# Kernel tuning notes

Hardware: AMD Instinct MI355X
Metric: run time of the kernel (lower is better)

The kernel has to match this reference:

```python
import jax, jax.numpy as jnp
import numpy as np

B, N, C_IN = 32, 1024, 128
F0, F1, F2 = 64, 64, 64
OUT = 10
RATIOS = (0.8, 0.8)
EPS = 1e-5


def setup_inputs() -> dict:
    key = jax.random.key(0)
    ks = jax.random.split(key, 16)
    N_nodes = jax.random.randint(ks[0], (B,), N // 2, N + 1)
    mask = (jnp.arange(N)[None, :] < N_nodes[:, None]).astype(jnp.float32)
    x = jax.random.normal(ks[1], (B, N, C_IN), dtype=jnp.float32)
    # sparse-ish symmetric binary adjacency restricted to valid nodes
    A = (jax.random.uniform(ks[2], (B, N, N)) < 0.02).astype(jnp.float32)
    A = jnp.maximum(A, jnp.swapaxes(A, 1, 2))
    A = A * mask[:, :, None] * mask[:, None, :]
    def lin(k, fi, fo):
        b = 1.0 / np.sqrt(fi)
        kw, kb = jax.random.split(k)
        return (jax.random.uniform(kw, (fi, fo), minval=-b, maxval=b),
                jax.random.uniform(kb, (fo,), minval=-b, maxval=b))
    W0, b0 = lin(ks[3], C_IN, F0)
    W1, b1 = lin(ks[4], F0, F1)
    W2, b2 = lin(ks[5], F1, F2)
    bp0 = 1.0 / np.sqrt(F0)
    p0 = jax.random.uniform(ks[6], (F0, 1), minval=-bp0, maxval=bp0)
    bp1 = 1.0 / np.sqrt(F1)
    p1 = jax.random.uniform(ks[7], (F1, 1), minval=-bp1, maxval=bp1)
    Wfc, bfc = lin(ks[8], F2, OUT)
    return {"x": x, "A": A, "mask": mask, "N_nodes": N_nodes,
            "W0": W0, "b0": b0, "W1": W1, "b1": b1, "W2": W2, "b2": b2,
            "p0": p0, "p1": p1, "Wfc": Wfc, "bfc": bfc}


def _gconv(x, A, W, b):
    # Kipf-Welling normalized Laplacian conv, batched dense
    n = A.shape[1]
    A_hat = A + jnp.eye(n, dtype=A.dtype)[None]
    D = (jnp.sum(A_hat, axis=1) + EPS) ** -0.5  # [B,N]
    L = D[:, :, None] * A_hat * D[:, None, :]
    h = jnp.einsum('bnm,bmc->bnc', L, x) @ W + b
    return jax.nn.relu(h)


def _pool(x, A, mask, N_nodes, p, ratio):
    Bc, Nc, C = x.shape
    y = (x.reshape(Bc * Nc, C) @ p).reshape(Bc, Nc)
    y = y / jnp.sqrt(jnp.sum(p ** 2))
    N_remove = (N_nodes.astype(jnp.float32) * (1.0 - ratio)).astype(N_nodes.dtype)
    # remove the N_remove lowest-scoring valid nodes per graph
    y_eff = jnp.where(mask > 0, y, jnp.inf)
    ranks = jnp.argsort(jnp.argsort(y_eff, axis=1), axis=1)  # ascending rank
    new_mask = mask * (ranks >= N_remove[:, None]).astype(mask.dtype)
    x = x * jnp.tanh(y)[:, :, None] * new_mask[:, :, None]
    A = new_mask[:, :, None] * A * new_mask[:, None, :]
    return x, A, new_mask, N_nodes - N_remove


def reference(x, A, mask, N_nodes, W0, b0, W1, b1, W2, b2, p0, p1, Wfc, bfc):
    x = _gconv(x, A, W0, b0)
    x, A, mask, N_nodes = _pool(x, A, mask, N_nodes, p0, RATIOS[0])
    x = _gconv(x, A, W1, b1)
    x, A, mask, N_nodes = _pool(x, A, mask, N_nodes, p1, RATIOS[1])
    x = _gconv(x, A, W2, b2)
    x = jnp.max(x, axis=1)  # global max pool over nodes [B,F2]
    return x @ Wfc + bfc
```

## Files before the change

kernel.cpp:

```cpp
#include <hip/hip_runtime.h>
#include <cstdint>
#include <cstddef>

#define BB 32
#define NN 1024
#define CIN 128
#define FF 64
#define NOUT 10
#define CAP 128
#define EPSV 1e-5f

typedef float vf4 __attribute__((ext_vector_type(4)));
__device__ __forceinline__ float4 ldnt(const float4* p) {
    vf4 v = __builtin_nontemporal_load((const vf4*)p);
    return make_float4(v.x, v.y, v.z, v.w);
}

__global__ __launch_bounds__(256) void k_front(const float* __restrict__ A,
                                               const float* __restrict__ x,
                                               const float* __restrict__ W0,
                                               const int* __restrict__ Nn,
                                               const float* __restrict__ b2f,
                                               float* __restrict__ gmax,
                                               unsigned short* __restrict__ adj,
                                               int* __restrict__ cnt,
                                               float* __restrict__ c1,
                                               float* __restrict__ c2,
                                               float* __restrict__ T) {
    __shared__ __align__(16) float Wl[64 * 64];
    int tid = threadIdx.x;
    int wave = tid >> 6, lane = tid & 63;
    if (blockIdx.x >= 10240) {
        for (int i = tid; i < BB * 64; i += 256)
            gmax[i] = fmaxf(b2f[i & 63], 0.f);
        return;
    }
    if (blockIdx.x >= 8192) {
        int gid = blockIdx.x - 8192;
        int b = gid & 31;
        int cch = gid >> 5;
        if (cch * 16 >= Nn[b]) return;
        int row0 = (b << 10) + cch * 16;
        int rsub = lane >> 4, f0 = (lane & 15) * 4;
        int r = row0 + wave * 4 + rsub;
        const float4* xr = (const float4*)(x + (size_t)r * CIN);
        float4 acc = {0.f, 0.f, 0.f, 0.f};
#pragma unroll
        for (int kc = 0; kc < 2; ++kc) {
            if (kc) __syncthreads();
            for (int t = tid; t < 64 * 16; t += 256)
                ((float4*)Wl)[t] = ((const float4*)W0)[kc * 1024 + t];
            __syncthreads();
#pragma unroll 4
            for (int k4 = 0; k4 < 16; ++k4) {
                float4 xv = ldnt(xr + kc * 16 + k4);
                float4 w0 = *(const float4*)&Wl[(k4 * 4 + 0) * 64 + f0];
                float4 w1 = *(const float4*)&Wl[(k4 * 4 + 1) * 64 + f0];
                float4 w2 = *(const float4*)&Wl[(k4 * 4 + 2) * 64 + f0];
                float4 w3 = *(const float4*)&Wl[(k4 * 4 + 3) * 64 + f0];
                acc.x += xv.x * w0.x; acc.y += xv.x * w0.y; acc.z += xv.x * w0.z; acc.w += xv.x * w0.w;
                acc.x += xv.y * w1.x; acc.y += xv.y * w1.y; acc.z += xv.y * w1.z; acc.w += xv.y * w1.w;
                acc.x += xv.z * w2.x; acc.y += xv.z * w2.y; acc.z += xv.z * w2.z; acc.w += xv.z * w2.w;
                acc.x += xv.w * w3.x; acc.y += xv.w * w3.y; acc.z += xv.w * w3.z; acc.w += xv.w * w3.w;
            }
        }
        *(float4*)&T[(size_t)r * 64 + f0] = acc;
    } else {
        int r = blockIdx.x * 4 + wave;
        int b = r >> 10;
        int Nb = Nn[b];
        int rl = r & 1023;
        if (rl >= Nb) {
            if (lane == 0) {
                cnt[r] = 0;
                float D = 1.0f / sqrtf(1.0f + EPSV);
                c1[r] = D;
                c2[r] = D * D;
            }
            return;
        }
        unsigned short* adjs = ((unsigned short*)Wl) + wave * CAP;
        const float4* Arow = (const float4*)(A + (size_t)r * NN);
        int nch = (Nb + 255) >> 8;
        float4 z4 = {0.f, 0.f, 0.f, 0.f};
        float4 v0 = ldnt(Arow + lane);
        float4 v1 = ldnt(Arow + 64 + lane);
        float4 v2 = (nch > 2) ? ldnt(Arow + 128 + lane) : z4;
        float4 v3 = (nch > 3) ? ldnt(Arow + 192 + lane) : z4;
        int c = 0;
        unsigned long long lt = (lane == 0) ? 0ULL : ((1ULL << lane) - 1ULL);
        float4 vv[4] = {v0, v1, v2, v3};
#pragma unroll
        for (int it = 0; it < 4; ++it) {
            float4 v = vv[it];
            int j0 = it * 256 + lane * 4;
            unsigned long long m0 = __ballot(v.x != 0.f);
            unsigned long long m1 = __ballot(v.y != 0.f);
            unsigned long long m2 = __ballot(v.z != 0.f);
            unsigned long long m3 = __ballot(v.w != 0.f);
            int before = __popcll(m0 & lt) + __popcll(m1 & lt) +
                         __popcll(m2 & lt) + __popcll(m3 & lt);
            int p = c + before;
            if (v.x != 0.f) { if (p < CAP) adjs[p] = (unsigned short)(j0 + 0); ++p; }
            if (v.y != 0.f) { if (p < CAP) adjs[p] = (unsigned short)(j0 + 1); ++p; }
            if (v.z != 0.f) { if (p < CAP) adjs[p] = (unsigned short)(j0 + 2); ++p; }
            if (v.w != 0.f) { if (p < CAP) adjs[p] = (unsigned short)(j0 + 3); ++p; }
            c += __popcll(m0) + __popcll(m1) + __popcll(m2) + __popcll(m3);
        }
        int cc = (c > CAP) ? CAP : c;
        uint32_t* dst = (uint32_t*)(adj + (size_t)r * CAP);
        if (lane * 2 < cc) dst[lane] = ((const uint32_t*)adjs)[lane];
        if (lane == 0) {
            cnt[r] = cc;
            float D = 1.0f / sqrtf((float)c + 1.0f + EPSV);
            c1[r] = D;
            c2[r] = D * D;
        }
    }
}

__global__ __launch_bounds__(256) void k_mid(const unsigned short* __restrict__ adj,
                                             const int* __restrict__ cnt,
                                             const float* __restrict__ nm,
                                             float* __restrict__ c1, float* __restrict__ c2,
                                             const float* __restrict__ Xin,
                                             const float* __restrict__ W,
                                             const float* __restrict__ y,
                                             float* __restrict__ T,
                                             const int* __restrict__ Nn) {
    __shared__ __align__(16) float Wl[64 * 64];
    int tid = threadIdx.x;
    if (blockIdx.x >= 8192) {
        int gid = blockIdx.x - 8192;
        int b = gid & 31;
        int cch = gid >> 5;
        if (cch * 16 >= Nn[b]) return;
        int row0 = (b << 10) + cch * 16;
        for (int t = tid; t < 64 * 16; t += 256)
            ((float4*)Wl)[t] = ((const float4*)W)[t];
        __syncthreads();
        int wave = tid >> 6, lane = tid & 63;
        int rsub = lane >> 4, f0 = (lane & 15) * 4;
        int r = row0 + wave * 4 + rsub;
        float sc = tanhf(y[r]) * nm[r];
        const float4* xr = (const float4*)(Xin + (size_t)r * 64);
        float4 acc = {0.f, 0.f, 0.f, 0.f};
#pragma unroll 4
        for (int k4 = 0; k4 < 16; ++k4) {
            float4 xv = ldnt(xr + k4);
            float4 w0 = *(const float4*)&Wl[(k4 * 4 + 0) * 64 + f0];
            float4 w1 = *(const float4*)&Wl[(k4 * 4 + 1) * 64 + f0];
            float4 w2 = *(const float4*)&Wl[(k4 * 4 + 2) * 64 + f0];
            float4 w3 = *(const float4*)&Wl[(k4 * 4 + 3) * 64 + f0];
            acc.x += xv.x * w0.x; acc.y += xv.x * w0.y; acc.z += xv.x * w0.z; acc.w += xv.x * w0.w;
            acc.x += xv.y * w1.x; acc.y += xv.y * w1.y; acc.z += xv.y * w1.z; acc.w += xv.y * w1.w;
            acc.x += xv.z * w2.x; acc.y += xv.z * w2.y; acc.z += xv.z * w2.z; acc.w += xv.z * w2.w;
            acc.x += xv.w * w3.x; acc.y += xv.w * w3.y; acc.z += xv.w * w3.z; acc.w += xv.w * w3.w;
        }
        acc.x *= sc; acc.y *= sc; acc.z *= sc; acc.w *= sc;
        *(float4*)&T[(size_t)r * 64 + f0] = acc;
    } else {
        int wave = tid >> 6, lane = tid & 63;
        int r = blockIdx.x * 4 + wave;
        int b = r >> 10;
        if ((r & 1023) >= Nn[b]) return;
        float m = nm[r];
        if (m == 0.f) {
            if (lane == 0) c1[r] = 0.f;
            return;
        }
        const unsigned short* arow = adj + (size_t)r * CAP;
        const float* nmb = nm + (b << 10);
        int n = cnt[r];
        float s = 0.f;
        if (lane < n)      s  = nmb[arow[lane]];
        if (lane + 64 < n) s += nmb[arow[lane + 64]];
        for (int sh = 32; sh; sh >>= 1) s += __shfl_xor(s, sh, 64);
        if (lane == 0) {
            float D = 1.0f / sqrtf(m * s + 1.0f + EPSV);
            c1[r] = m * D;
            c2[r] = D * D;
        }
    }
}

__global__ __launch_bounds__(256) void k_spmm(const unsigned short* __restrict__ adj,
                                              const int* __restrict__ cnt,
                                              const float* __restrict__ c1,
                                              const float* __restrict__ c2,
                                              const float* __restrict__ T,
                                              const float* __restrict__ bias,
                                              float* __restrict__ X,
                                              const float* __restrict__ p,
                                              float* __restrict__ y,
                                              float* __restrict__ gmax,
                                              const int* __restrict__ Nn) {
    __shared__ __align__(16) float c1s[NN];
    __shared__ float red[4][64];
    int b   = blockIdx.x & 31;
    int cch = blockIdx.x >> 5;
    int Nb = Nn[b];
    if (cch * 16 >= Nb) return;
    int tid = threadIdx.x;
    int n4 = (Nb + 3) >> 2;
    if (tid < n4) ((float4*)c1s)[tid] = ((const float4*)(c1 + (b << 10)))[tid];
    __syncthreads();
    int wave = tid >> 6, lane = tid & 63;
    int r0 = (b << 10) + cch * 16 + wave * 4;
    const float* Tb = T + ((size_t)(b << 10) << 6);
    float bv = bias[lane];
    float pv = 0.f, ppinv = 0.f;
    if (p != nullptr) {
        pv = p[lane];
        float pp = pv * pv;
        for (int s = 32; s; s >>= 1) pp += __shfl_xor(pp, s, 64);
        ppinv = 1.0f / sqrtf(pp);
    }
    float vmax = 0.f;
#pragma unroll
    for (int rr = 0; rr < 4; ++rr) {
        int r = r0 + rr;
        int rl = r & 1023;
        if (rl >= Nb) break;
        if (c1s[rl] == 0.f) continue;
        const unsigned short* arow = adj + (size_t)r * CAP;
        int n = cnt[r];
        float acc0 = 0.f, acc1 = 0.f, acc2 = 0.f, acc3 = 0.f;
        int t = 0;
        for (; t + 4 <= n; t += 4) {
            ushort4 j4 = *(const ushort4*)(arow + t);
            acc0 += c1s[j4.x] * Tb[((int)j4.x << 6) + lane];
            acc1 += c1s[j4.y] * Tb[((int)j4.y << 6) + lane];
            acc2 += c1s[j4.z] * Tb[((int)j4.z << 6) + lane];
            acc3 += c1s[j4.w] * Tb[((int)j4.w << 6) + lane];
        }
        for (; t < n; ++t) {
            int j = arow[t];
            acc0 += c1s[j] * Tb[(j << 6) + lane];
        }
        float acc = (acc0 + acc1) + (acc2 + acc3);
        float o = c1s[rl] * acc + c2[r] * T[((size_t)r << 6) + lane] + bv;
        o = fmaxf(o, 0.f);
        if (X != nullptr) X[((size_t)r << 6) + lane] = o;
        if (p != nullptr) {
            float a = o * pv;
            for (int s = 32; s; s >>= 1) a += __shfl_xor(a, s, 64);
            if (lane == 0) y[r] = a * ppinv;
        }
        vmax = fmaxf(vmax, o);
    }
    if (gmax != nullptr) {
        red[wave][lane] = vmax;
        __syncthreads();
        if (wave == 0) {
            float m = fmaxf(fmaxf(red[0][lane], red[1][lane]),
                            fmaxf(red[2][lane], red[3][lane]));
            atomicMax((int*)&gmax[(b << 6) + lane], __float_as_int(m));
        }
    }
}

__global__ __launch_bounds__(256) void k_rank(const float* __restrict__ y,
                                              const float* __restrict__ maskSrc,
                                              const int* __restrict__ nsrc,
                                              const int* __restrict__ nbound,
                                              float* __restrict__ nmOut,
                                              int* __restrict__ ncur) {
    __shared__ __align__(16) float yv[NN];
    int b = blockIdx.x >> 4;
    int sub = blockIdx.x & 15;
    int tid = threadIdx.x;
    const float INF = __builtin_inff();
    int Nb = nbound[b];
    if ((sub << 6) >= Nb) return;
    {
        float4 v;
        if (tid * 4 < Nb) {
            v = ((const float4*)(y + (b << 10)))[tid];
            float4 m = ((const float4*)(maskSrc + (b << 10)))[tid];
            v.x = (m.x > 0.f) ? v.x : INF;
            v.y = (m.y > 0.f) ? v.y : INF;
            v.z = (m.z > 0.f) ? v.z : INF;
            v.w = (m.w > 0.f) ? v.w : INF;
        } else {
            v.x = INF; v.y = INF; v.z = INF; v.w = INF;
        }
        ((float4*)yv)[tid] = v;
    }
    int n = nsrc[b];
    const float RM = (float)(1.0 - 0.8);
    int nrem = (int)((float)n * RM);
    if (sub == 0 && tid == 0) ncur[b] = n - nrem;
    __syncthreads();
    int i = (sub << 6) + (tid >> 2);
    int q = tid & 3;
    float yi = yv[i];
    int rank = 0;
    if (yi < INF) {
        const float4* jbase = (const float4*)yv + (q << 6);
        int j0 = q << 8;
        int tend = (Nb - j0 + 3) >> 2;
        if (tend > 64) tend = 64;
#pragma unroll 8
        for (int t = 0; t < tend; ++t) {
            float4 a = jbase[t];
            int j = j0 + t * 4;
            rank += (a.x < yi || (a.x == yi && j     < i)) ? 1 : 0;
            rank += (a.y < yi || (a.y == yi && j + 1 < i)) ? 1 : 0;
            rank += (a.z < yi || (a.z == yi && j + 2 < i)) ? 1 : 0;
            rank += (a.w < yi || (a.w == yi && j + 3 < i)) ? 1 : 0;
        }
    }
    rank += __shfl_xor(rank, 1, 64);
    rank += __shfl_xor(rank, 2, 64);
    if (q == 0) {
        float nmv = (yi < INF && rank >= nrem) ? 1.f : 0.f;
        nmOut[(b << 10) + i] = nmv;
    }
}

__global__ __launch_bounds__(64) void k_fc(const float* __restrict__ gmax,
                                           const float* __restrict__ Wfc,
                                           const float* __restrict__ bfc,
                                           float* __restrict__ out) {
    __shared__ float gl[64];
    int b = blockIdx.x, lane = threadIdx.x;
    gl[lane] = gmax[(b << 6) + lane];
    __syncthreads();
    if (lane < NOUT) {
        float acc = bfc[lane];
        for (int k = 0; k < 64; ++k) acc += gl[k] * Wfc[k * NOUT + lane];
        out[b * NOUT + lane] = acc;
    }
}

extern "C" void kernel_launch(void* const* d_in, const int* in_sizes, int n_in,
                              void* d_out, int out_size, void* d_ws, size_t ws_size,
                              hipStream_t stream) {
    const float* x    = (const float*)d_in[0];
    const float* A    = (const float*)d_in[1];
    const float* mask = (const float*)d_in[2];
    const int*   Nn   = (const int*)d_in[3];
    const float* W0   = (const float*)d_in[4];
    const float* b0   = (const float*)d_in[5];
    const float* W1   = (const float*)d_in[6];
    const float* b1   = (const float*)d_in[7];
    const float* W2   = (const float*)d_in[8];
    const float* b2   = (const float*)d_in[9];
    const float* p0   = (const float*)d_in[10];
    const float* p1   = (const float*)d_in[11];
    const float* Wfc  = (const float*)d_in[12];
    const float* bfc  = (const float*)d_in[13];
    float* out = (float*)d_out;

    char* ws = (char*)d_ws;
    size_t off = 0;
    auto alloc = [&](size_t bytes) -> void* {
        void* p = ws + off;
        off = (off + bytes + 255) & ~(size_t)255;
        return p;
    };
    unsigned short* adj = (unsigned short*)alloc((size_t)BB * NN * CAP * 2);
    int*   cnt  = (int*)  alloc((size_t)BB * NN * 4);
    float* X    = (float*)alloc((size_t)BB * NN * 64 * 4);
    float* T    = (float*)alloc((size_t)BB * NN * 64 * 4);
    float* c1   = (float*)alloc((size_t)BB * NN * 4);
    float* c2   = (float*)alloc((size_t)BB * NN * 4);
    float* y    = (float*)alloc((size_t)BB * NN * 4);
    float* nm0  = (float*)alloc((size_t)BB * NN * 4);
    float* nm1  = (float*)alloc((size_t)BB * NN * 4);
    int*   nc0  = (int*)  alloc((size_t)BB * 4);
    int*   nc1  = (int*)  alloc((size_t)BB * 4);
    float* gmax = (float*)alloc((size_t)BB * 64 * 4);

    k_front<<<8192 + 2048 + 1, 256, 0, stream>>>(A, x, W0, Nn, b2, gmax,
                                                 adj, cnt, c1, c2, T);
    k_spmm<<<2048, 256, 0, stream>>>(adj, cnt, c1, c2, T, b0, X, p0, y, nullptr, Nn);
    k_rank<<<BB * 16, 256, 0, stream>>>(y, mask, Nn, Nn, nm0, nc0);
    k_mid<<<8192 + 2048, 256, 0, stream>>>(adj, cnt, nm0, c1, c2, X, W1, y, T, Nn);
    k_spmm<<<2048, 256, 0, stream>>>(adj, cnt, c1, c2, T, b1, X, p1, y, nullptr, Nn);
    k_rank<<<BB * 16, 256, 0, stream>>>(y, nm0, nc0, Nn, nm1, nc1);
    k_mid<<<8192 + 2048, 256, 0, stream>>>(adj, cnt, nm1, c1, c2, X, W2, y, T, Nn);
    k_spmm<<<2048, 256, 0, stream>>>(adj, cnt, c1, c2, T, b2, nullptr, nullptr, nullptr,
                                     gmax, Nn);
    k_fc<<<BB, 64, 0, stream>>>(gmax, Wfc, bfc, out);
}
```

Measured before the change: 355.1 us.

## Fuse rank and FC into spmm via last-block-per-graph atomic counter

Removes the separate k_rank and k_fc launches. Each k_spmm block now bumps a per-graph counter, and the last block to finish for a graph computes the top-k mask or the final FC layer in place. Ranking switches to packed 64-bit sortable keys with a single block doing an O(N^2) comparison per graph, where the old k_rank spread this over 16 blocks. This saves launch gaps but serialises the ranking work onto one block per graph.

```diff
diff --git a/kernel.cpp b/kernel.cpp
--- a/kernel.cpp
+++ b/kernel.cpp
@@ -26,13 +26,15 @@
                                                int* __restrict__ cnt,
                                                float* __restrict__ c1,
                                                float* __restrict__ c2,
-                                               float* __restrict__ T) {
+                                               float* __restrict__ T,
+                                               int* __restrict__ ctrs) {
     __shared__ __align__(16) float Wl[64 * 64];
     int tid = threadIdx.x;
     int wave = tid >> 6, lane = tid & 63;
     if (blockIdx.x >= 10240) {
         for (int i = tid; i < BB * 64; i += 256)
             gmax[i] = fmaxf(b2f[i & 63], 0.f);
+        if (tid < 96) ctrs[tid] = 0;
         return;
     }
     if (blockIdx.x >= 8192) {
@@ -194,9 +196,19 @@
                                               const float* __restrict__ p,
                                               float* __restrict__ y,
                                               float* __restrict__ gmax,
-                                              const int* __restrict__ Nn) {
+                                              const int* __restrict__ Nn,
+                                              const float* __restrict__ maskSrc,
+                                              const int* __restrict__ nsrc,
+                                              float* __restrict__ nmOut,
+                                              int* __restrict__ ncur,
+                                              const float* __restrict__ Wfc,
+                                              const float* __restrict__ bfc,
+                                              float* __restrict__ outP,
+                                              int* __restrict__ ctr) {
     __shared__ __align__(16) float c1s[NN];
+    __shared__ __align__(16) unsigned long long kv[NN];
     __shared__ float red[4][64];
+    __shared__ int islast;
     int b   = blockIdx.x & 31;
     int cch = blockIdx.x >> 5;
     int Nb = Nn[b];
@@ -258,79 +270,77 @@
             atomicMax((int*)&gmax[(b << 6) + lane], __float_as_int(m));
         }
     }
-}
-
-__global__ __launch_bounds__(256) void k_rank(const float* __restrict__ y,
-                                              const float* __restrict__ maskSrc,
-                                              const int* __restrict__ nsrc,
-                                              const int* __restrict__ nbound,
-                                              float* __restrict__ nmOut,
-                                              int* __restrict__ ncur) {
-    __shared__ __align__(16) float yv[NN];
-    int b = blockIdx.x >> 4;
-    int sub = blockIdx.x & 15;
-    int tid = threadIdx.x;
+    __syncthreads();
+    if (tid == 0) {
+        __threadfence();
+        int target = (Nb + 15) >> 4;
+        int old = __hip_atomic_fetch_add(&ctr[b], 1, __ATOMIC_ACQ_REL,
+                                         __HIP_MEMORY_SCOPE_AGENT);
+        islast = (old == target - 1);
+    }
+    __syncthreads();
+    if (!islast) return;
+    __threadfence();
     const float INF = __builtin_inff();
-    int Nb = nbound[b];
-    if ((sub << 6) >= Nb) return;
-    {
-        float4 v;
-        if (tid * 4 < Nb) {
-            v = ((const float4*)(y + (b << 10)))[tid];
-            float4 m = ((const float4*)(maskSrc + (b << 10)))[tid];
-            v.x = (m.x > 0.f) ? v.x : INF;
-            v.y = (m.y > 0.f) ? v.y : INF;
-            v.z = (m.z > 0.f) ? v.z : INF;
-            v.w = (m.w > 0.f) ? v.w : INF;
-        } else {
-            v.x = INF; v.y = INF; v.z = INF; v.w = INF;
-        }
-        ((float4*)yv)[tid] = v;
-    }
-    int n = nsrc[b];
-    const float RM = (float)(1.0 - 0.8);
-    int nrem = (int)((float)n * RM);
-    if (sub == 0 && tid == 0) ncur[b] = n - nrem;
-    __syncthreads();
-    int i = (sub << 6) + (tid >> 2);
-    int q = tid & 3;
-    float yi = yv[i];
-    int rank = 0;
-    if (yi < INF) {
-        const float4* jbase = (const float4*)yv + (q << 6);
-        int j0 = q << 8;
-        int tend = (Nb - j0 + 3) >> 2;
-        if (tend > 64) tend = 64;
-#pragma unroll 8
-        for (int t = 0; t < tend; ++t) {
-            float4 a = jbase[t];
-            int j = j0 + t * 4;
-            rank += (a.x < yi || (a.x == yi && j     < i)) ? 1 : 0;
-            rank += (a.y < yi || (a.y == yi && j + 1 < i)) ? 1 : 0;
-            rank += (a.z < yi || (a.z == yi && j + 2 < i)) ? 1 : 0;
-            rank += (a.w < yi || (a.w == yi && j + 3 < i)) ? 1 : 0;
-        }
-    }
-    rank += __shfl_xor(rank, 1, 64);
-    rank += __shfl_xor(rank, 2, 64);
-    if (q == 0) {
-        float nmv = (yi < INF && rank >= nrem) ? 1.f : 0.f;
-        nmOut[(b << 10) + i] = nmv;
-    }
-}
-
-__global__ __launch_bounds__(64) void k_fc(const float* __restrict__ gmax,
-                                           const float* __restrict__ Wfc,
-                                           const float* __restrict__ bfc,
-                                           float* __restrict__ out) {
-    __shared__ float gl[64];
-    int b = blockIdx.x, lane = threadIdx.x;
-    gl[lane] = gmax[(b << 6) + lane];
-    __syncthreads();
-    if (lane < NOUT) {
-        float acc = bfc[lane];
-        for (int k = 0; k < 64; ++k) acc += gl[k] * Wfc[k * NOUT + lane];
-        out[b * NOUT + lane] = acc;
+    if (nmOut != nullptr) {
+        float* yv = c1s;
+        {
+            float4 v;
+            if (tid * 4 < Nb) {
+                v = ((const float4*)(y + (b << 10)))[tid];
+                float4 m = ((const float4*)(maskSrc + (b << 10)))[tid];
+                v.x = (m.x > 0.f) ? v.x : INF;
+                v.y = (m.y > 0.f) ? v.y : INF;
+                v.z = (m.z > 0.f) ? v.z : INF;
+                v.w = (m.w > 0.f) ? v.w : INF;
+            } else {
+                v.x = INF; v.y = INF; v.z = INF; v.w = INF;
+            }
+            ((float4*)yv)[tid] = v;
+        }
+        int n = nsrc[b];
+        const float RM = (float)(1.0 - 0.8);
+        int nrem = (int)((float)n * RM);
+        if (tid == 0) ncur[b] = n - nrem;
+        __syncthreads();
+#pragma unroll
+        for (int t = 0; t < 4; ++t) {
+            int i = tid + (t << 8);
+            unsigned int u = __float_as_uint(yv[i]);
+            u ^= (unsigned int)((int)u >> 31) | 0x80000000u;
+            kv[i] = ((unsigned long long)u << 10) | (unsigned int)i;
+        }
+        __syncthreads();
+        unsigned long long k0 = kv[tid], k1 = kv[tid + 256],
+                           k2 = kv[tid + 512], k3 = kv[tid + 768];
+        int r0k = 0, r1k = 0, r2k = 0, r3k = 0;
+        int nkc = (Nb + 1) >> 1;
+#pragma unroll 4
+        for (int c = 0; c < nkc; ++c) {
+            ulonglong2 a = ((const ulonglong2*)kv)[c];
+            r0k += (a.x < k0) + (a.y < k0);
+            r1k += (a.x < k1) + (a.y < k1);
+            r2k += (a.x < k2) + (a.y < k2);
+            r3k += (a.x < k3) + (a.y < k3);
+        }
+        int rk[4] = {r0k, r1k, r2k, r3k};
+#pragma unroll
+        for (int t = 0; t < 4; ++t) {
+            int i = tid + (t << 8);
+            nmOut[(b << 10) + i] = (yv[i] < INF && rk[t] >= nrem) ? 1.f : 0.f;
+        }
+    } else if (outP != nullptr) {
+        float* gl = c1s;
+        if (tid < 64)
+            gl[tid] = __uint_as_float(__hip_atomic_load(
+                (unsigned int*)&gmax[(b << 6) + tid],
+                __ATOMIC_RELAXED, __HIP_MEMORY_SCOPE_AGENT));
+        __syncthreads();
+        if (tid < NOUT) {
+            float acc = bfc[tid];
+            for (int k = 0; k < 64; ++k) acc += gl[k] * Wfc[k * NOUT + tid];
+            outP[b * NOUT + tid] = acc;
+        }
     }
 }
 
@@ -372,16 +382,20 @@
     int*   nc0  = (int*)  alloc((size_t)BB * 4);
     int*   nc1  = (int*)  alloc((size_t)BB * 4);
     float* gmax = (float*)alloc((size_t)BB * 64 * 4);
+    int*   ctrs = (int*)  alloc(96 * 4);
 
     k_front<<<8192 + 2048 + 1, 256, 0, stream>>>(A, x, W0, Nn, b2, gmax,
-                                                 adj, cnt, c1, c2, T);
-    k_spmm<<<2048, 256, 0, stream>>>(adj, cnt, c1, c2, T, b0, X, p0, y, nullptr, Nn);
-    k_rank<<<BB * 16, 256, 0, stream>>>(y, mask, Nn, Nn, nm0, nc0);
+                                                 adj, cnt, c1, c2, T, ctrs);
+    k_spmm<<<2048, 256, 0, stream>>>(adj, cnt, c1, c2, T, b0, X, p0, y, nullptr, Nn,
+                                     mask, Nn, nm0, nc0,
+                                     nullptr, nullptr, nullptr, ctrs);
     k_mid<<<8192 + 2048, 256, 0, stream>>>(adj, cnt, nm0, c1, c2, X, W1, y, T, Nn);
-    k_spmm<<<2048, 256, 0, stream>>>(adj, cnt, c1, c2, T, b1, X, p1, y, nullptr, Nn);
-    k_rank<<<BB * 16, 256, 0, stream>>>(y, nm0, nc0, Nn, nm1, nc1);
+    k_spmm<<<2048, 256, 0, stream>>>(adj, cnt, c1, c2, T, b1, X, p1, y, nullptr, Nn,
+                                     nm0, nc0, nm1, nc1,
+                                     nullptr, nullptr, nullptr, ctrs + 32);
     k_mid<<<8192 + 2048, 256, 0, stream>>>(adj, cnt, nm1, c1, c2, X, W2, y, T, Nn);
     k_spmm<<<2048, 256, 0, stream>>>(adj, cnt, c1, c2, T, b2, nullptr, nullptr, nullptr,
-                                     gmax, Nn);
-    k_fc<<<BB, 64, 0, stream>>>(gmax, Wfc, bfc, out);
+                                     gmax, Nn,
+                                     nullptr, nullptr, nullptr, nullptr,
+                                     Wfc, bfc, out, ctrs + 64);
 }
```

New measurement: 566.4 us. +59.5%, slower.

## Fuse rank and mask-degree computation into GEMM kernel, defer tanh scaling to SpMM

Applied to the files above, without the earlier changes.

The separate pooling rank kernel is merged with the degree/normalisation pass and launched in the same grid as the feature GEMM, which removes two kernel launches and their dependency stalls. Each rank block now recomputes ranks for the whole graph using packed 64-bit (key, index) comparisons, so it can build the new mask in shared memory for neighbour degree sums. The tanh(y)·mask scaling is no longer applied to T in the GEMM but per-neighbour inside the SpMM gather. The cost is redundant rank work across the sixteen sub-blocks of each graph and extra shared-memory loads and multiplies in the SpMM inner loop.

```diff
diff --git a/kernel.cpp b/kernel.cpp
--- a/kernel.cpp
+++ b/kernel.cpp
@@ -119,19 +119,120 @@
     }
 }
 
-__global__ __launch_bounds__(256) void k_mid(const unsigned short* __restrict__ adj,
-                                             const int* __restrict__ cnt,
-                                             const float* __restrict__ nm,
-                                             float* __restrict__ c1, float* __restrict__ c2,
-                                             const float* __restrict__ Xin,
-                                             const float* __restrict__ W,
-                                             const float* __restrict__ y,
-                                             float* __restrict__ T,
-                                             const int* __restrict__ Nn) {
-    __shared__ __align__(16) float Wl[64 * 64];
+template<int DEFER>
+__global__ __launch_bounds__(256) void k_spmm(const unsigned short* __restrict__ adj,
+                                              const int* __restrict__ cnt,
+                                              const float* __restrict__ c1,
+                                              const float* __restrict__ c2,
+                                              const float* __restrict__ T,
+                                              const float* __restrict__ bias,
+                                              float* __restrict__ X,
+                                              const float* __restrict__ p,
+                                              float* __restrict__ y,
+                                              float* __restrict__ gmax,
+                                              const int* __restrict__ Nn,
+                                              const float* __restrict__ scs) {
+    __shared__ __align__(16) float c1s[NN];
+    __shared__ __align__(16) float scss[DEFER ? NN : 4];
+    __shared__ float red[4][64];
+    int b   = blockIdx.x & 31;
+    int cch = blockIdx.x >> 5;
+    int Nb = Nn[b];
+    if (cch * 16 >= Nb) return;
     int tid = threadIdx.x;
-    if (blockIdx.x >= 8192) {
-        int gid = blockIdx.x - 8192;
+    int n4 = (Nb + 3) >> 2;
+    if (tid < n4) {
+        ((float4*)c1s)[tid] = ((const float4*)(c1 + (b << 10)))[tid];
+        if (DEFER)
+            ((float4*)scss)[tid] = ((const float4*)(scs + (b << 10)))[tid];
+    }
+    __syncthreads();
+    int wave = tid >> 6, lane = tid & 63;
+    int r0 = (b << 10) + cch * 16 + wave * 4;
+    const float* Tb = T + ((size_t)(b << 10) << 6);
+    float bv = bias[lane];
+    float pv = 0.f, ppinv = 0.f;
+    if (p != nullptr) {
+        pv = p[lane];
+        float pp = pv * pv;
+        for (int s = 32; s; s >>= 1) pp += __shfl_xor(pp, s, 64);
+        ppinv = 1.0f / sqrtf(pp);
+    }
+    float vmax = 0.f;
+#pragma unroll
+    for (int rr = 0; rr < 4; ++rr) {
+        int r = r0 + rr;
+        int rl = r & 1023;
+        if (rl >= Nb) break;
+        if (DEFER && c1s[rl] == 0.f) continue;
+        const unsigned short* arow = adj + (size_t)r * CAP;
+        int n = cnt[r];
+        float acc0 = 0.f, acc1 = 0.f, acc2 = 0.f, acc3 = 0.f;
+        int t = 0;
+        for (; t + 4 <= n; t += 4) {
+            ushort4 j4 = *(const ushort4*)(arow + t);
+            float t0 = Tb[((int)j4.x << 6) + lane];
+            float t1 = Tb[((int)j4.y << 6) + lane];
+            float t2 = Tb[((int)j4.z << 6) + lane];
+            float t3 = Tb[((int)j4.w << 6) + lane];
+            if (DEFER) {
+                t0 *= scss[j4.x]; t1 *= scss[j4.y];
+                t2 *= scss[j4.z]; t3 *= scss[j4.w];
+            }
+            acc0 += c1s[j4.x] * t0;
+            acc1 += c1s[j4.y] * t1;
+            acc2 += c1s[j4.z] * t2;
+            acc3 += c1s[j4.w] * t3;
+        }
+        for (; t < n; ++t) {
+            int j = arow[t];
+            float tv = Tb[(j << 6) + lane];
+            if (DEFER) tv *= scss[j];
+            acc0 += c1s[j] * tv;
+        }
+        float acc = (acc0 + acc1) + (acc2 + acc3);
+        float selfT = T[((size_t)r << 6) + lane];
+        if (DEFER) selfT = scss[rl] * selfT;
+        float o = c1s[rl] * acc + c2[r] * selfT + bv;
+        o = fmaxf(o, 0.f);
+        if (X != nullptr) X[((size_t)r << 6) + lane] = o;
+        if (p != nullptr) {
+            float a = o * pv;
+            for (int s = 32; s; s >>= 1) a += __shfl_xor(a, s, 64);
+            if (lane == 0) y[r] = a * ppinv;
+        }
+        vmax = fmaxf(vmax, o);
+    }
+    if (gmax != nullptr) {
+        red[wave][lane] = vmax;
+        __syncthreads();
+        if (wave == 0) {
+            float m = fmaxf(fmaxf(red[0][lane], red[1][lane]),
+                            fmaxf(red[2][lane], red[3][lane]));
+            atomicMax((int*)&gmax[(b << 6) + lane], __float_as_int(m));
+        }
+    }
+}
+
+__global__ __launch_bounds__(256) void k_rankgemm(const float* __restrict__ y,
+                                                  const float* __restrict__ maskSrc,
+                                                  const int* __restrict__ nsrc,
+                                                  const int* __restrict__ Nn,
+                                                  const unsigned short* __restrict__ adj,
+                                                  const int* __restrict__ cnt,
+                                                  const float* __restrict__ Xin,
+                                                  const float* __restrict__ W,
+                                                  float* __restrict__ nmOut,
+                                                  int* __restrict__ ncur,
+                                                  float* __restrict__ c1o,
+                                                  float* __restrict__ c2o,
+                                                  float* __restrict__ scso,
+                                                  float* __restrict__ T) {
+    __shared__ __align__(16) char smem[16384];
+    int tid = threadIdx.x;
+    if (blockIdx.x >= 512) {
+        float* Wl = (float*)smem;
+        int gid = blockIdx.x - 512;
         int b = gid & 31;
         int cch = gid >> 5;
         if (cch * 16 >= Nn[b]) return;
@@ -142,7 +243,6 @@
         int wave = tid >> 6, lane = tid & 63;
         int rsub = lane >> 4, f0 = (lane & 15) * 4;
         int r = row0 + wave * 4 + rsub;
-        float sc = tanhf(y[r]) * nm[r];
         const float4* xr = (const float4*)(Xin + (size_t)r * 64);
         float4 acc = {0.f, 0.f, 0.f, 0.f};
 #pragma unroll 4
@@ -157,165 +257,93 @@
             acc.x += xv.z * w2.x; acc.y += xv.z * w2.y; acc.z += xv.z * w2.z; acc.w += xv.z * w2.w;
             acc.x += xv.w * w3.x; acc.y += xv.w * w3.y; acc.z += xv.w * w3.z; acc.w += xv.w * w3.w;
         }
-        acc.x *= sc; acc.y *= sc; acc.z *= sc; acc.w *= sc;
         *(float4*)&T[(size_t)r * 64 + f0] = acc;
     } else {
+        float* yv = (float*)smem;
+        unsigned long long* kv = (unsigned long long*)(smem + 4096);
+        float* nml = (float*)(smem + 12288);
+        int b = blockIdx.x >> 4;
+        int sub = blockIdx.x & 15;
+        const float INF = __builtin_inff();
+        int Nb = Nn[b];
+        if ((sub << 6) >= Nb) return;
+        {
+            float4 v;
+            if (tid * 4 < Nb) {
+                v = ((const float4*)(y + (b << 10)))[tid];
+                float4 m = ((const float4*)(maskSrc + (b << 10)))[tid];
+                v.x = (m.x > 0.f) ? v.x : INF;
+                v.y = (m.y > 0.f) ? v.y : INF;
+                v.z = (m.z > 0.f) ? v.z : INF;
+                v.w = (m.w > 0.f) ? v.w : INF;
+            } else {
+                v.x = INF; v.y = INF; v.z = INF; v.w = INF;
+            }
+            ((float4*)yv)[tid] = v;
+        }
+        int n = nsrc[b];
+        const float RM = (float)(1.0 - 0.8);
+        int nrem = (int)((float)n * RM);
+        if (sub == 0 && tid == 0) ncur[b] = n - nrem;
+        __syncthreads();
+#pragma unroll
+        for (int t = 0; t < 4; ++t) {
+            int i = tid + (t << 8);
+            unsigned int u = __float_as_uint(yv[i]);
+            u ^= (unsigned int)((int)u >> 31) | 0x80000000u;
+            kv[i] = ((unsigned long long)u << 10) | (unsigned int)i;
+        }
+        __syncthreads();
+        unsigned long long k0 = kv[tid], k1 = kv[tid + 256],
+                           k2 = kv[tid + 512], k3 = kv[tid + 768];
+        int r0 = 0, r1 = 0, r2 = 0, r3 = 0;
+        int nkc = (Nb + 1) >> 1;
+#pragma unroll 4
+        for (int c = 0; c < nkc; ++c) {
+            ulonglong2 a = ((const ulonglong2*)kv)[c];
+            r0 += (a.x < k0) + (a.y < k0);
+            r1 += (a.x < k1) + (a.y < k1);
+            r2 += (a.x < k2) + (a.y < k2);
+            r3 += (a.x < k3) + (a.y < k3);
+        }
+        int rk[4] = {r0, r1, r2, r3};
+#pragma unroll
+        for (int t = 0; t < 4; ++t) {
+            int i = tid + (t << 8);
+            nml[i] = (yv[i] < INF && rk[t] >= nrem) ? 1.f : 0.f;
+        }
+        __syncthreads();
         int wave = tid >> 6, lane = tid & 63;
-        int r = blockIdx.x * 4 + wave;
-        int b = r >> 10;
-        if ((r & 1023) >= Nn[b]) return;
-        float m = nm[r];
-        if (m == 0.f) {
-            if (lane == 0) c1[r] = 0.f;
-            return;
-        }
-        const unsigned short* arow = adj + (size_t)r * CAP;
-        const float* nmb = nm + (b << 10);
-        int n = cnt[r];
-        float s = 0.f;
-        if (lane < n)      s  = nmb[arow[lane]];
-        if (lane + 64 < n) s += nmb[arow[lane + 64]];
-        for (int sh = 32; sh; sh >>= 1) s += __shfl_xor(s, sh, 64);
-        if (lane == 0) {
-            float D = 1.0f / sqrtf(m * s + 1.0f + EPSV);
-            c1[r] = m * D;
-            c2[r] = D * D;
-        }
-    }
-}
-
-__global__ __launch_bounds__(256) void k_spmm(const unsigned short* __restrict__ adj,
-                                              const int* __restrict__ cnt,
-                                              const float* __restrict__ c1,
-                                              const float* __restrict__ c2,
-                                              const float* __restrict__ T,
-                                              const float* __restrict__ bias,
-                                              float* __restrict__ X,
-                                              const float* __restrict__ p,
-                                              float* __restrict__ y,
-                                              float* __restrict__ gmax,
-                                              const int* __restrict__ Nn) {
-    __shared__ __align__(16) float c1s[NN];
-    __shared__ float red[4][64];
-    int b   = blockIdx.x & 31;
-    int cch = blockIdx.x >> 5;
-    int Nb = Nn[b];
-    if (cch * 16 >= Nb) return;
-    int tid = threadIdx.x;
-    int n4 = (Nb + 3) >> 2;
-    if (tid < n4) ((float4*)c1s)[tid] = ((const float4*)(c1 + (b << 10)))[tid];
-    __syncthreads();
-    int wave = tid >> 6, lane = tid & 63;
-    int r0 = (b << 10) + cch * 16 + wave * 4;
-    const float* Tb = T + ((size_t)(b << 10) << 6);
-    float bv = bias[lane];
-    float pv = 0.f, ppinv = 0.f;
-    if (p != nullptr) {
-        pv = p[lane];
-        float pp = pv * pv;
-        for (int s = 32; s; s >>= 1) pp += __shfl_xor(pp, s, 64);
-        ppinv = 1.0f / sqrtf(pp);
-    }
-    float vmax = 0.f;
-#pragma unroll
-    for (int rr = 0; rr < 4; ++rr) {
-        int r = r0 + rr;
-        int rl = r & 1023;
-        if (rl >= Nb) break;
-        if (c1s[rl] == 0.f) continue;
-        const unsigned short* arow = adj + (size_t)r * CAP;
-        int n = cnt[r];
-        float acc0 = 0.f, acc1 = 0.f, acc2 = 0.f, acc3 = 0.f;
-        int t = 0;
-        for (; t + 4 <= n; t += 4) {
-            ushort4 j4 = *(const ushort4*)(arow + t);
-            acc0 += c1s[j4.x] * Tb[((int)j4.x << 6) + lane];
-            acc1 += c1s[j4.y] * Tb[((int)j4.y << 6) + lane];
-            acc2 += c1s[j4.z] * Tb[((int)j4.z << 6) + lane];
-            acc3 += c1s[j4.w] * Tb[((int)j4.w << 6) + lane];
-        }
-        for (; t < n; ++t) {
-            int j = arow[t];
-            acc0 += c1s[j] * Tb[(j << 6) + lane];
-        }
-        float acc = (acc0 + acc1) + (acc2 + acc3);
-        float o = c1s[rl] * acc + c2[r] * T[((size_t)r << 6) + lane] + bv;
-        o = fmaxf(o, 0.f);
-        if (X != nullptr) X[((size_t)r << 6) + lane] = o;
-        if (p != nullptr) {
-            float a = o * pv;
-            for (int s = 32; s; s >>= 1) a += __shfl_xor(a, s, 64);
-            if (lane == 0) y[r] = a * ppinv;
-        }
-        vmax = fmaxf(vmax, o);
-    }
-    if (gmax != nullptr) {
-        red[wave][lane] = vmax;
-        __syncthreads();
-        if (wave == 0) {
-            float m = fmaxf(fmaxf(red[0][lane], red[1][lane]),
-                            fmaxf(red[2][lane], red[3][lane]));
-            atomicMax((int*)&gmax[(b << 6) + lane], __float_as_int(m));
-        }
-    }
-}
-
-__global__ __launch_bounds__(256) void k_rank(const float* __restrict__ y,
-                                              const float* __restrict__ maskSrc,
-                                              const int* __restrict__ nsrc,
-                                              const int* __restrict__ nbound,
-                                              float* __restrict__ nmOut,
-                                              int* __restrict__ ncur) {
-    __shared__ __align__(16) float yv[NN];
-    int b = blockIdx.x >> 4;
-    int sub = blockIdx.x & 15;
-    int tid = threadIdx.x;
-    const float INF = __builtin_inff();
-    int Nb = nbound[b];
-    if ((sub << 6) >= Nb) return;
-    {
-        float4 v;
-        if (tid * 4 < Nb) {
-            v = ((const float4*)(y + (b << 10)))[tid];
-            float4 m = ((const float4*)(maskSrc + (b << 10)))[tid];
-            v.x = (m.x > 0.f) ? v.x : INF;
-            v.y = (m.y > 0.f) ? v.y : INF;
-            v.z = (m.z > 0.f) ? v.z : INF;
-            v.w = (m.w > 0.f) ? v.w : INF;
-        } else {
-            v.x = INF; v.y = INF; v.z = INF; v.w = INF;
-        }
-        ((float4*)yv)[tid] = v;
-    }
-    int n = nsrc[b];
-    const float RM = (float)(1.0 - 0.8);
-    int nrem = (int)((float)n * RM);
-    if (sub == 0 && tid == 0) ncur[b] = n - nrem;
-    __syncthreads();
-    int i = (sub << 6) + (tid >> 2);
-    int q = tid & 3;
-    float yi = yv[i];
-    int rank = 0;
-    if (yi < INF) {
-        const float4* jbase = (const float4*)yv + (q << 6);
-        int j0 = q << 8;
-        int tend = (Nb - j0 + 3) >> 2;
-        if (tend > 64) tend = 64;
-#pragma unroll 8
-        for (int t = 0; t < tend; ++t) {
-            float4 a = jbase[t];
-            int j = j0 + t * 4;
-            rank += (a.x < yi || (a.x == yi && j     < i)) ? 1 : 0;
-            rank += (a.y < yi || (a.y == yi && j + 1 < i)) ? 1 : 0;
-            rank += (a.z < yi || (a.z == yi && j + 2 < i)) ? 1 : 0;
-            rank += (a.w < yi || (a.w == yi && j + 3 < i)) ? 1 : 0;
-        }
-    }
-    rank += __shfl_xor(rank, 1, 64);
-    rank += __shfl_xor(rank, 2, 64);
-    if (q == 0) {
-        float nmv = (yi < INF && rank >= nrem) ? 1.f : 0.f;
-        nmOut[(b << 10) + i] = nmv;
+        for (int rd = 0; rd < 16; ++rd) {
+            int i = (sub << 6) + (rd << 2) + wave;
+            int gr = (b << 10) + i;
+            if (i >= Nb) {
+                if (lane == 0) nmOut[gr] = 0.f;
+                continue;
+            }
+            float m = nml[i];
+            if (m == 0.f) {
+                if (lane == 0) {
+                    nmOut[gr] = 0.f;
+                    c1o[gr] = 0.f;
+                    scso[gr] = 0.f;
+                }
+                continue;
+            }
+            int nn = cnt[gr];
+            const unsigned short* ar = adj + (size_t)gr * CAP;
+            float s = 0.f;
+            if (lane < nn)      s  = nml[ar[lane]];
+            if (lane + 64 < nn) s += nml[ar[lane + 64]];
+            for (int sh = 32; sh; sh >>= 1) s += __shfl_xor(s, sh, 64);
+            if (lane == 0) {
+                nmOut[gr] = 1.f;
+                float D = 1.0f / sqrtf(m * s + 1.0f + EPSV);
+                c1o[gr] = m * D;
+                c2o[gr] = D * D;
+                scso[gr] = tanhf(yv[i]) * m;
+            }
+        }
     }
 }
 
@@ -366,6 +394,7 @@
     float* T    = (float*)alloc((size_t)BB * NN * 64 * 4);
     float* c1   = (float*)alloc((size_t)BB * NN * 4);
     float* c2   = (float*)alloc((size_t)BB * NN * 4);
+    float* scs  = (float*)alloc((size_t)BB * NN * 4);
     float* y    = (float*)alloc((size_t)BB * NN * 4);
     float* nm0  = (float*)alloc((size_t)BB * NN * 4);
     float* nm1  = (float*)alloc((size_t)BB * NN * 4);
@@ -375,13 +404,15 @@
 
     k_front<<<8192 + 2048 + 1, 256, 0, stream>>>(A, x, W0, Nn, b2, gmax,
                                                  adj, cnt, c1, c2, T);
-    k_spmm<<<2048, 256, 0, stream>>>(adj, cnt, c1, c2, T, b0, X, p0, y, nullptr, Nn);
-    k_rank<<<BB * 16, 256, 0, stream>>>(y, mask, Nn, Nn, nm0, nc0);
-    k_mid<<<8192 + 2048, 256, 0, stream>>>(adj, cnt, nm0, c1, c2, X, W1, y, T, Nn);
-    k_spmm<<<2048, 256, 0, stream>>>(adj, cnt, c1, c2, T, b1, X, p1, y, nullptr, Nn);
-    k_rank<<<BB * 16, 256, 0, stream>>>(y, nm0, nc0, Nn, nm1, nc1);
-    k_mid<<<8192 + 2048, 256, 0, stream>>>(adj, cnt, nm1, c1, c2, X, W2, y, T, Nn);
-    k_spmm<<<2048, 256, 0, stream>>>(adj, cnt, c1, c2, T, b2, nullptr, nullptr, nullptr,
-                                     gmax, Nn);
+    k_spmm<0><<<2048, 256, 0, stream>>>(adj, cnt, c1, c2, T, b0, X, p0, y,
+                                        nullptr, Nn, nullptr);
+    k_rankgemm<<<512 + 2048, 256, 0, stream>>>(y, mask, Nn, Nn, adj, cnt, X, W1,
+                                               nm0, nc0, c1, c2, scs, T);
+    k_spmm<1><<<2048, 256, 0, stream>>>(adj, cnt, c1, c2, T, b1, X, p1, y,
+                                        nullptr, Nn, scs);
+    k_rankgemm<<<512 + 2048, 256, 0, stream>>>(y, nm0, nc0, Nn, adj, cnt, X, W2,
+                                               nm1, nc1, c1, c2, scs, T);
+    k_spmm<1><<<2048, 256, 0, stream>>>(adj, cnt, c1, c2, T, b2, nullptr, nullptr,
+                                        nullptr, gmax, Nn, scs);
     k_fc<<<BB, 64, 0, stream>>>(gmax, Wfc, bfc, out);
 }
```

Result: slower. 402.4 us (+13.3%).
